# Optimization experiments

Measured on AMD Instinct MI355X. Metric: run time of the kernel, lower is better.

## Reference

```python
import jax, jax.numpy as jnp
import numpy as np

L, DIRS, FEAT, H, B, T = 2, 2, 512, 256, 64, 1024  # layers, directions, feat_dim, per-dir hidden, n_trees, chain_len


def setup_inputs() -> dict:
    key = jax.random.key(0)
    ks = jax.random.split(key, 4)
    s = 0.05
    features = jax.random.normal(ks[0], (B, T, FEAT), jnp.float32)
    Wx = jax.random.normal(ks[1], (L, DIRS, FEAT, 5 * H), jnp.float32) * s
    bx = jnp.zeros((L, DIRS, 5 * H), jnp.float32)
    Wh = jax.random.normal(ks[2], (L, DIRS, H, 5 * H), jnp.float32) * s
    # forget-gate bias slice [2H:3H] initialized to 1.0 as in ChainLSTM
    bh = jnp.zeros((L, DIRS, 5 * H), jnp.float32).at[:, :, 2 * H:3 * H].set(1.0)
    Wp = jax.random.normal(ks[3], (L, DIRS, FEAT, H), jnp.float32) * s
    bp = jnp.zeros((L, DIRS, H), jnp.float32)
    return dict(features=features, Wx=Wx, bx=bx, Wh=Wh, bh=bh, Wp=Wp, bp=bp)


def _run_direction(x, Wx_d, bx_d, Wh_d, bh_d, Wp_d, bp_d, reverse):
    # x: [T, B, F]. Precompute input projections as one big GEMM (memory-bound stream),
    # then scan only carries the tiny [B,H] @ [H,5H] recurrence.
    gx = x @ Wx_d + bx_d          # [T, B, 5H]
    px = x @ Wp_d + bp_d          # [T, B, H] highway projection

    def step(carry, inp):
        c, h = carry
        g, p = inp
        z = g + h @ Wh_d + bh_d
        i, o, f, u, r = jnp.split(z, 5, axis=-1)
        c = jax.nn.sigmoid(i) * jnp.tanh(u) + jax.nn.sigmoid(f) * c
        hh = jax.nn.sigmoid(o) * jnp.tanh(c)
        rg = jax.nn.sigmoid(r)
        hf = rg * hh + (1.0 - rg) * p  # highway gate
        return (c, hf), hf

    zero = jnp.zeros((x.shape[1], bh_d.shape[-1] // 5), x.dtype)
    _, hs = jax.lax.scan(step, (zero, zero), (gx, px), reverse=reverse)
    return hs  # [T, B, H], aligned to original node positions


def reference(features, Wx, bx, Wh, bh, Wp, bp):
    x = jnp.swapaxes(features, 0, 1)  # [T, B, F]
    n_layers = Wx.shape[0]
    for l in range(n_layers):
        outs = []
        for d in range(Wx.shape[1]):  # 0 = foreward, 1 = backward
            hs = _run_direction(x, Wx[l, d], bx[l, d], Wh[l, d], bh[l, d],
                                Wp[l, d], bp[l, d], reverse=(d == 1))
            outs.append(hs)
        x = jnp.concatenate(outs, axis=-1)  # [T, B, 2H] -> next layer input
    return jnp.swapaxes(x, 0, 1)  # [B, T, 2H]
```

## Files before the change

### kernel.cpp

```cpp
#include <hip/hip_runtime.h>
#include <hip/hip_bf16.h>

#define LAYERS 2
#define DIRS   2
#define FEAT   512
#define HDIM   256
#define BATCH  64
#define TLEN   1024
#define FIVEH  1280
#define CHUNK  64
#define NCHUNK (TLEN / CHUNK)
#define NW     8

typedef short bf16x8 __attribute__((ext_vector_type(8)));
typedef float f32x4  __attribute__((ext_vector_type(4)));

__device__ __forceinline__ unsigned short f2bf(float x) {
    unsigned u = __float_as_uint(x);
    unsigned r = (u + 0x7fffu + ((u >> 16) & 1u)) >> 16;
    return (unsigned short)r;
}
__device__ __forceinline__ float bf2f(unsigned short h) {
    return __uint_as_float(((unsigned)h) << 16);
}
__device__ __forceinline__ float sigf(float x) {
    return 1.0f / (1.0f + __expf(-x));
}
__device__ __forceinline__ float tanhfast(float x) {
    return 1.0f - 2.0f / (__expf(2.0f * x) + 1.0f);
}

__global__ __launch_bounds__(256) void castT_kernel(
    const float* __restrict__ src, unsigned short* __restrict__ dst, int K, int N)
{
    __shared__ float tile[32][33];
    const int n0 = blockIdx.x * 32, k0 = blockIdx.y * 32;
    const size_t slab = (size_t)blockIdx.z * K * N;
    src += slab; dst += slab;
    const int tx = threadIdx.x & 31, ty = threadIdx.x >> 5;
    #pragma unroll
    for (int r = 0; r < 32; r += 8)
        tile[ty + r][tx] = src[(size_t)(k0 + ty + r) * N + (n0 + tx)];
    __syncthreads();
    #pragma unroll
    for (int r = 0; r < 32; r += 8)
        dst[(size_t)(n0 + ty + r) * K + (k0 + tx)] = f2bf(tile[tx][ty + r]);
}

__global__ __launch_bounds__(64) void init_kernel(int* __restrict__ flags) {
    if (threadIdx.x < 2 * NW) flags[threadIdx.x * 16] = 0;
}

__global__ __launch_bounds__(256) void proj_kernel(
    const float* __restrict__ features,
    const unsigned short* __restrict__ x1,
    const unsigned short* __restrict__ Wx_t,
    const unsigned short* __restrict__ Wp_t,
    const float* __restrict__ bx, const float* __restrict__ bh,
    const float* __restrict__ bp,
    unsigned short* __restrict__ gx_c,
    unsigned short* __restrict__ px_c,
    int layer, int chunk)
{
    const int ntb = blockIdx.x;
    const int mt  = blockIdx.y;
    const int d   = blockIdx.z;
    const int tid = threadIdx.x;
    const int wave = tid >> 6, lane = tid & 63;

    __shared__ __align__(16) unsigned short Alds[64][40];
    __shared__ __align__(16) unsigned short Blds[64][40];

    const int n0 = ntb * 64;
    const bool isWx = (n0 < FIVEH);
    const unsigned short* Wt = isWx
        ? (Wx_t + ((size_t)(layer * 2 + d) * FIVEH + n0) * FEAT)
        : (Wp_t + ((size_t)(layer * 2 + d) * HDIM + (n0 - FIVEH)) * FEAT);

    const int m0 = mt * 64;
    const int lm = tid >> 2;
    const int lkb = tid & 3;

    const int mrow = m0 + lm;
    const int tl = mrow >> 6;
    const int b  = mrow & 63;
    const int tglob = (d == 0) ? (chunk * CHUNK + tl) : (TLEN - 1 - (chunk * CHUNK + tl));
    const float* Arow0 = features + ((size_t)b * TLEN + tglob) * FEAT;
    const unsigned short* Arow1 = x1 + ((size_t)tglob * BATCH + b) * FEAT;

    f32x4 acc[4];
    #pragma unroll
    for (int i = 0; i < 4; ++i) acc[i] = 0.0f;

    const int fr = lane & 15, quad = lane >> 4;

    for (int k0 = 0; k0 < FEAT; k0 += 32) {
        if (layer == 0) {
            float4 a0 = *(const float4*)(Arow0 + k0 + lkb * 8);
            float4 a1 = *(const float4*)(Arow0 + k0 + lkb * 8 + 4);
            unsigned short* dst = &Alds[lm][lkb * 8];
            dst[0] = f2bf(a0.x); dst[1] = f2bf(a0.y);
            dst[2] = f2bf(a0.z); dst[3] = f2bf(a0.w);
            dst[4] = f2bf(a1.x); dst[5] = f2bf(a1.y);
            dst[6] = f2bf(a1.z); dst[7] = f2bf(a1.w);
        } else {
            uint4 a = *(const uint4*)(Arow1 + k0 + lkb * 8);
            *(uint4*)&Alds[lm][lkb * 8] = a;
        }
        uint4 bv = *(const uint4*)(Wt + (size_t)lm * FEAT + k0 + lkb * 8);
        *(uint4*)&Blds[lm][lkb * 8] = bv;
        __syncthreads();

        bf16x8 af = *(const bf16x8*)&Alds[wave * 16 + fr][quad * 8];
        #pragma unroll
        for (int nt = 0; nt < 4; ++nt) {
            bf16x8 bf = *(const bf16x8*)&Blds[nt * 16 + fr][quad * 8];
            acc[nt] = __builtin_amdgcn_mfma_f32_16x16x32_bf16(af, bf, acc[nt], 0, 0, 0);
        }
        __syncthreads();
    }

    const int ldoff = layer * 2 + d;
    #pragma unroll
    for (int nt = 0; nt < 4; ++nt) {
        const int n = n0 + nt * 16 + fr;
        #pragma unroll
        for (int r = 0; r < 4; ++r) {
            const int m2 = m0 + wave * 16 + quad * 4 + r;
            const int tl2 = m2 >> 6, b2 = m2 & 63;
            float v = acc[nt][r];
            if (n < FIVEH) {
                v += bx[(size_t)ldoff * FIVEH + n] + bh[(size_t)ldoff * FIVEH + n];
                const int g = n >> 8, j = n & 255;
                gx_c[((((size_t)d * CHUNK + tl2) * 5 + g) * HDIM + j) * BATCH + b2] = f2bf(v);
            } else {
                const int j = n - FIVEH;
                v += bp[(size_t)ldoff * HDIM + j];
                px_c[(((size_t)d * CHUNK + tl2) * HDIM + j) * BATCH + b2] = f2bf(v);
            }
        }
    }
}

__global__ __launch_bounds__(256, 1) void recur_kernel(
    const unsigned short* __restrict__ gx_c,
    const unsigned short* __restrict__ px_c,
    const unsigned short* __restrict__ Wh_t,
    unsigned short* __restrict__ x1,
    float* __restrict__ out,
    float* __restrict__ cbuf,
    unsigned short* __restrict__ hbuf,
    int* __restrict__ flags,
    int layer, int chunk)
{
    const int blk = blockIdx.x;
    const int d = blk >> 3, wg = blk & 7;
    const int tid = threadIdx.x;
    const int wave = tid >> 6, lane = tid & 63;
    const int mw = wave >> 1, jh = wave & 1;
    const int col = lane & 15, quad = lane >> 4;
    const int jg = wg * 32 + jh * 16 + col;

    bf16x8 bfr[5][8];
    const unsigned short* Wb = Wh_t + (size_t)(layer * 2 + d) * FIVEH * HDIM;
    #pragma unroll
    for (int g = 0; g < 5; ++g)
        #pragma unroll
        for (int ks = 0; ks < 8; ++ks)
            bfr[g][ks] = *(const bf16x8*)(Wb + (size_t)(g * HDIM + jg) * HDIM + ks * 32 + quad * 8);

    float cst[2][4];
    #pragma unroll
    for (int mt = 0; mt < 2; ++mt)
        #pragma unroll
        for (int r = 0; r < 4; ++r) {
            const int b = (2 * mw + mt) * 16 + quad * 4 + r;
            cst[mt][r] = (chunk == 0) ? 0.0f
                       : cbuf[((size_t)d * BATCH + b) * HDIM + jg];
        }

    const int base = layer * TLEN + chunk * CHUNK;
    int* myflag = &flags[(d * NW + wg) * 16];

    for (int s = 0; s < CHUNK; ++s) {
        const int gs = base + s;

        if (tid < NW) {
            while (__hip_atomic_load(&flags[(d * NW + tid) * 16],
                                     __ATOMIC_RELAXED, __HIP_MEMORY_SCOPE_AGENT) < gs) { }
        }
        __syncthreads();
        __threadfence();

        f32x4 acc[2][5];
        #pragma unroll
        for (int mt = 0; mt < 2; ++mt)
            #pragma unroll
            for (int g = 0; g < 5; ++g) acc[mt][g] = 0.0f;

        if ((gs & (TLEN - 1)) != 0) {
            const unsigned short* hs = hbuf + (size_t)(((gs + 1) & 1) * 2 + d) * BATCH * HDIM;
            bf16x8 af[2][8];
            #pragma unroll
            for (int mt = 0; mt < 2; ++mt)
                #pragma unroll
                for (int ks = 0; ks < 8; ++ks)
                    af[mt][ks] = *(const bf16x8*)(hs + (size_t)((2 * mw + mt) * 16 + col) * HDIM
                                                  + ks * 32 + quad * 8);
            #pragma unroll
            for (int ks = 0; ks < 8; ++ks)
                #pragma unroll
                for (int g = 0; g < 5; ++g) {
                    acc[0][g] = __builtin_amdgcn_mfma_f32_16x16x32_bf16(af[0][ks], bfr[g][ks], acc[0][g], 0, 0, 0);
                    acc[1][g] = __builtin_amdgcn_mfma_f32_16x16x32_bf16(af[1][ks], bfr[g][ks], acc[1][g], 0, 0, 0);
                }
        }

        ushort4 gxv[2][5], pxv[2];
        #pragma unroll
        for (int mt = 0; mt < 2; ++mt) {
            const size_t bb = (2 * mw + mt) * 16 + quad * 4;
            #pragma unroll
            for (int g = 0; g < 5; ++g)
                gxv[mt][g] = *(const ushort4*)(gx_c + ((((size_t)d * CHUNK + s) * 5 + g) * HDIM + jg) * BATCH + bb);
            pxv[mt] = *(const ushort4*)(px_c + (((size_t)d * CHUNK + s) * HDIM + jg) * BATCH + bb);
        }

        const int tpos = chunk * CHUNK + s;
        const int tglob = d ? (TLEN - 1 - tpos) : tpos;
        unsigned short* hdst = hbuf + (size_t)((gs & 1) * 2 + d) * BATCH * HDIM;

        #pragma unroll
        for (int mt = 0; mt < 2; ++mt) {
            const unsigned short* gq0 = (const unsigned short*)&gxv[mt][0];
            const unsigned short* gq1 = (const unsigned short*)&gxv[mt][1];
            const unsigned short* gq2 = (const unsigned short*)&gxv[mt][2];
            const unsigned short* gq3 = (const unsigned short*)&gxv[mt][3];
            const unsigned short* gq4 = (const unsigned short*)&gxv[mt][4];
            const unsigned short* pq  = (const unsigned short*)&pxv[mt];
            #pragma unroll
            for (int r = 0; r < 4; ++r) {
                const float z0 = acc[mt][0][r] + bf2f(gq0[r]);
                const float z1 = acc[mt][1][r] + bf2f(gq1[r]);
                const float z2 = acc[mt][2][r] + bf2f(gq2[r]);
                const float z3 = acc[mt][3][r] + bf2f(gq3[r]);
                const float z4 = acc[mt][4][r] + bf2f(gq4[r]);
                const float p  = bf2f(pq[r]);
                const float ig = sigf(z0);
                const float og = sigf(z1);
                const float fg = sigf(z2);
                const float ug = tanhfast(z3);
                const float rg = sigf(z4);
                const float cc = ig * ug + fg * cst[mt][r];
                cst[mt][r] = cc;
                const float hh = og * tanhfast(cc);
                const float h = rg * hh + (1.0f - rg) * p;
                const int b = (2 * mw + mt) * 16 + quad * 4 + r;
                hdst[(size_t)b * HDIM + jg] = f2bf(h);
                if (layer == 0)
                    x1[((size_t)tglob * BATCH + b) * 512 + d * HDIM + jg] = f2bf(h);
                else
                    out[((size_t)b * TLEN + tglob) * 512 + d * HDIM + jg] = h;
            }
        }

        __syncthreads();
        if (tid == 0) {
            __threadfence();
            __hip_atomic_store(myflag, gs + 1, __ATOMIC_RELAXED, __HIP_MEMORY_SCOPE_AGENT);
        }
    }

    #pragma unroll
    for (int mt = 0; mt < 2; ++mt)
        #pragma unroll
        for (int r = 0; r < 4; ++r) {
            const int b = (2 * mw + mt) * 16 + quad * 4 + r;
            cbuf[((size_t)d * BATCH + b) * HDIM + jg] = cst[mt][r];
        }
}

extern "C" void kernel_launch(void* const* d_in, const int* in_sizes, int n_in,
                              void* d_out, int out_size, void* d_ws, size_t ws_size,
                              hipStream_t stream) {
    const float* features = (const float*)d_in[0];
    const float* Wx = (const float*)d_in[1];
    const float* bx = (const float*)d_in[2];
    const float* Wh = (const float*)d_in[3];
    const float* bh = (const float*)d_in[4];
    const float* Wp = (const float*)d_in[5];
    const float* bp = (const float*)d_in[6];
    float* out = (float*)d_out;

    char* ws = (char*)d_ws;
    size_t off = 0;
    auto alloc = [&](size_t bytes) -> void* {
        void* p = ws + off;
        off += (bytes + 255) & ~(size_t)255;
        return p;
    };
    unsigned short* Wx_t = (unsigned short*)alloc((size_t)LAYERS * DIRS * FIVEH * FEAT * 2);
    unsigned short* Wh_t = (unsigned short*)alloc((size_t)LAYERS * DIRS * FIVEH * HDIM * 2);
    unsigned short* Wp_t = (unsigned short*)alloc((size_t)LAYERS * DIRS * HDIM * FEAT * 2);
    unsigned short* x1   = (unsigned short*)alloc((size_t)TLEN * BATCH * 512 * 2);
    unsigned short* gx_c = (unsigned short*)alloc((size_t)DIRS * CHUNK * BATCH * FIVEH * 2);
    unsigned short* px_c = (unsigned short*)alloc((size_t)DIRS * CHUNK * BATCH * HDIM * 2);
    float* cbuf = (float*)alloc((size_t)DIRS * BATCH * HDIM * 4);
    unsigned short* hbuf = (unsigned short*)alloc((size_t)2 * DIRS * BATCH * HDIM * 2);
    int* flags = (int*)alloc((size_t)2 * NW * 16 * 4);

    init_kernel<<<1, 64, 0, stream>>>(flags);
    castT_kernel<<<dim3(FIVEH / 32, FEAT / 32, 4), 256, 0, stream>>>(Wx, Wx_t, FEAT, FIVEH);
    castT_kernel<<<dim3(FIVEH / 32, HDIM / 32, 4), 256, 0, stream>>>(Wh, Wh_t, HDIM, FIVEH);
    castT_kernel<<<dim3(HDIM / 32, FEAT / 32, 4), 256, 0, stream>>>(Wp, Wp_t, FEAT, HDIM);

    for (int l = 0; l < LAYERS; ++l) {
        for (int c = 0; c < NCHUNK; ++c) {
            proj_kernel<<<dim3(24, 64, 2), 256, 0, stream>>>(
                features, x1, Wx_t, Wp_t, bx, bh, bp, gx_c, px_c, l, c);
            recur_kernel<<<DIRS * NW, 256, 0, stream>>>(
                gx_c, px_c, Wh_t, x1, out, cbuf, hbuf, flags, l, c);
        }
    }
}
```

Measured before the change: 17.65 ms.

## Stage h tile in LDS, publish via atomic stores, hoist gx loads before spin

Each block first writes its bf16 hidden-state slice into a shared-memory tile, then publishes it to the global ping-pong buffer with coalesced 64-bit relaxed atomic stores. The consumer side reads h through atomic loads, and both __threadfence calls are dropped. The gx/px loads are moved ahead of the spin-wait so their latency overlaps the wait. This cuts per-step fence cost and scattered 2-byte global stores, but relies on relaxed agent-scope atomics plus __syncthreads for ordering, which is subtle and could allow stale reads.

```diff
diff --git a/kernel.cpp b/kernel.cpp
--- a/kernel.cpp
+++ b/kernel.cpp
@@ -14,6 +14,9 @@
 
 typedef short bf16x8 __attribute__((ext_vector_type(8)));
 typedef float f32x4  __attribute__((ext_vector_type(4)));
+
+#define ALOAD(p)    __hip_atomic_load((p),      __ATOMIC_RELAXED, __HIP_MEMORY_SCOPE_AGENT)
+#define ASTORE(p,v) __hip_atomic_store((p),(v), __ATOMIC_RELAXED, __HIP_MEMORY_SCOPE_AGENT)
 
 __device__ __forceinline__ unsigned short f2bf(float x) {
     unsigned u = __float_as_uint(x);
@@ -161,6 +164,8 @@
     const int col = lane & 15, quad = lane >> 4;
     const int jg = wg * 32 + jh * 16 + col;
 
+    __shared__ __align__(16) unsigned short hlds[BATCH][32];
+
     bf16x8 bfr[5][8];
     const unsigned short* Wb = Wh_t + (size_t)(layer * 2 + d) * FIVEH * HDIM;
     #pragma unroll
@@ -185,12 +190,20 @@
     for (int s = 0; s < CHUNK; ++s) {
         const int gs = base + s;
 
+        ushort4 gxv[2][5], pxv[2];
+        #pragma unroll
+        for (int mt = 0; mt < 2; ++mt) {
+            const size_t bb = (2 * mw + mt) * 16 + quad * 4;
+            #pragma unroll
+            for (int g = 0; g < 5; ++g)
+                gxv[mt][g] = *(const ushort4*)(gx_c + ((((size_t)d * CHUNK + s) * 5 + g) * HDIM + jg) * BATCH + bb);
+            pxv[mt] = *(const ushort4*)(px_c + (((size_t)d * CHUNK + s) * HDIM + jg) * BATCH + bb);
+        }
+
         if (tid < NW) {
-            while (__hip_atomic_load(&flags[(d * NW + tid) * 16],
-                                     __ATOMIC_RELAXED, __HIP_MEMORY_SCOPE_AGENT) < gs) { }
-        }
-        __syncthreads();
-        __threadfence();
+            while (ALOAD(&flags[(d * NW + tid) * 16]) < gs) { }
+        }
+        __syncthreads();
 
         f32x4 acc[2][5];
         #pragma unroll
@@ -199,14 +212,20 @@
             for (int g = 0; g < 5; ++g) acc[mt][g] = 0.0f;
 
         if ((gs & (TLEN - 1)) != 0) {
-            const unsigned short* hs = hbuf + (size_t)(((gs + 1) & 1) * 2 + d) * BATCH * HDIM;
+            const unsigned long long* hs = (const unsigned long long*)
+                (hbuf + (size_t)(((gs + 1) & 1) * 2 + d) * BATCH * HDIM);
             bf16x8 af[2][8];
             #pragma unroll
             for (int mt = 0; mt < 2; ++mt)
                 #pragma unroll
-                for (int ks = 0; ks < 8; ++ks)
-                    af[mt][ks] = *(const bf16x8*)(hs + (size_t)((2 * mw + mt) * 16 + col) * HDIM
-                                                  + ks * 32 + quad * 8);
+                for (int ks = 0; ks < 8; ++ks) {
+                    const size_t o = ((size_t)((2 * mw + mt) * 16 + col) * HDIM
+                                      + ks * 32 + quad * 8) >> 2;
+                    union { unsigned long long q[2]; bf16x8 v; } u;
+                    u.q[0] = ALOAD(hs + o);
+                    u.q[1] = ALOAD(hs + o + 1);
+                    af[mt][ks] = u.v;
+                }
             #pragma unroll
             for (int ks = 0; ks < 8; ++ks)
                 #pragma unroll
@@ -216,19 +235,8 @@
                 }
         }
 
-        ushort4 gxv[2][5], pxv[2];
-        #pragma unroll
-        for (int mt = 0; mt < 2; ++mt) {
-            const size_t bb = (2 * mw + mt) * 16 + quad * 4;
-            #pragma unroll
-            for (int g = 0; g < 5; ++g)
-                gxv[mt][g] = *(const ushort4*)(gx_c + ((((size_t)d * CHUNK + s) * 5 + g) * HDIM + jg) * BATCH + bb);
-            pxv[mt] = *(const ushort4*)(px_c + (((size_t)d * CHUNK + s) * HDIM + jg) * BATCH + bb);
-        }
-
         const int tpos = chunk * CHUNK + s;
         const int tglob = d ? (TLEN - 1 - tpos) : tpos;
-        unsigned short* hdst = hbuf + (size_t)((gs & 1) * 2 + d) * BATCH * HDIM;
 
         #pragma unroll
         for (int mt = 0; mt < 2; ++mt) {
@@ -256,19 +264,30 @@
                 const float hh = og * tanhfast(cc);
                 const float h = rg * hh + (1.0f - rg) * p;
                 const int b = (2 * mw + mt) * 16 + quad * 4 + r;
-                hdst[(size_t)b * HDIM + jg] = f2bf(h);
+                const unsigned short hb = f2bf(h);
+                hlds[b][jh * 16 + col] = hb;
                 if (layer == 0)
-                    x1[((size_t)tglob * BATCH + b) * 512 + d * HDIM + jg] = f2bf(h);
+                    x1[((size_t)tglob * BATCH + b) * 512 + d * HDIM + jg] = hb;
                 else
                     out[((size_t)b * TLEN + tglob) * 512 + d * HDIM + jg] = h;
             }
         }
 
         __syncthreads();
-        if (tid == 0) {
-            __threadfence();
-            __hip_atomic_store(myflag, gs + 1, __ATOMIC_RELAXED, __HIP_MEMORY_SCOPE_AGENT);
-        }
+
+        {
+            const int b = tid >> 2, jo = (tid & 3) * 8;
+            unsigned long long* hd = (unsigned long long*)
+                (hbuf + (size_t)((gs & 1) * 2 + d) * BATCH * HDIM)
+                + (((size_t)b * HDIM + wg * 32 + jo) >> 2);
+            const unsigned long long* hsv = (const unsigned long long*)&hlds[b][jo];
+            ASTORE(hd,     hsv[0]);
+            ASTORE(hd + 1, hsv[1]);
+        }
+
+        __syncthreads();
+        if (tid == 0)
+            ASTORE(myflag, gs + 1);
     }
 
     #pragma unroll
```

After: 18.95 ms. 1.07x slower.

## Replace flag barrier with step-tagged hidden-state words polled per element

Applied to the files above, without the earlier changes.

Each hidden-state value is now stored as a 32-bit word holding the bf16 value plus the 16-bit step index. Consumers poll those words directly with relaxed atomics until every tag matches the expected step. This removes the per-step flag spin, __syncthreads and thread fences, and lets the gx/px loads be issued before the wait. In exchange the hbuf traffic doubles. A retry guard can fall through and use stale data, and leftover tags from an earlier launch can match the expected step, which makes correctness depend on timing.

```diff
diff --git a/kernel.cpp b/kernel.cpp
--- a/kernel.cpp
+++ b/kernel.cpp
@@ -11,9 +11,14 @@
 #define CHUNK  64
 #define NCHUNK (TLEN / CHUNK)
 #define NW     8
+#define RETRY_GUARD 2048
 
 typedef short bf16x8 __attribute__((ext_vector_type(8)));
 typedef float f32x4  __attribute__((ext_vector_type(4)));
+typedef unsigned long long u64;
+
+#define ALOAD(p)    __hip_atomic_load((p),      __ATOMIC_RELAXED, __HIP_MEMORY_SCOPE_AGENT)
+#define ASTORE(p,v) __hip_atomic_store((p),(v), __ATOMIC_RELAXED, __HIP_MEMORY_SCOPE_AGENT)
 
 __device__ __forceinline__ unsigned short f2bf(float x) {
     unsigned u = __float_as_uint(x);
@@ -45,10 +50,6 @@
     #pragma unroll
     for (int r = 0; r < 32; r += 8)
         dst[(size_t)(n0 + ty + r) * K + (k0 + tx)] = f2bf(tile[tx][ty + r]);
-}
-
-__global__ __launch_bounds__(64) void init_kernel(int* __restrict__ flags) {
-    if (threadIdx.x < 2 * NW) flags[threadIdx.x * 16] = 0;
 }
 
 __global__ __launch_bounds__(256) void proj_kernel(
@@ -149,8 +150,7 @@
     unsigned short* __restrict__ x1,
     float* __restrict__ out,
     float* __restrict__ cbuf,
-    unsigned short* __restrict__ hbuf,
-    int* __restrict__ flags,
+    unsigned int* __restrict__ hbuf,
     int layer, int chunk)
 {
     const int blk = blockIdx.x;
@@ -180,41 +180,9 @@
         }
 
     const int base = layer * TLEN + chunk * CHUNK;
-    int* myflag = &flags[(d * NW + wg) * 16];
 
     for (int s = 0; s < CHUNK; ++s) {
         const int gs = base + s;
-
-        if (tid < NW) {
-            while (__hip_atomic_load(&flags[(d * NW + tid) * 16],
-                                     __ATOMIC_RELAXED, __HIP_MEMORY_SCOPE_AGENT) < gs) { }
-        }
-        __syncthreads();
-        __threadfence();
-
-        f32x4 acc[2][5];
-        #pragma unroll
-        for (int mt = 0; mt < 2; ++mt)
-            #pragma unroll
-            for (int g = 0; g < 5; ++g) acc[mt][g] = 0.0f;
-
-        if ((gs & (TLEN - 1)) != 0) {
-            const unsigned short* hs = hbuf + (size_t)(((gs + 1) & 1) * 2 + d) * BATCH * HDIM;
-            bf16x8 af[2][8];
-            #pragma unroll
-            for (int mt = 0; mt < 2; ++mt)
-                #pragma unroll
-                for (int ks = 0; ks < 8; ++ks)
-                    af[mt][ks] = *(const bf16x8*)(hs + (size_t)((2 * mw + mt) * 16 + col) * HDIM
-                                                  + ks * 32 + quad * 8);
-            #pragma unroll
-            for (int ks = 0; ks < 8; ++ks)
-                #pragma unroll
-                for (int g = 0; g < 5; ++g) {
-                    acc[0][g] = __builtin_amdgcn_mfma_f32_16x16x32_bf16(af[0][ks], bfr[g][ks], acc[0][g], 0, 0, 0);
-                    acc[1][g] = __builtin_amdgcn_mfma_f32_16x16x32_bf16(af[1][ks], bfr[g][ks], acc[1][g], 0, 0, 0);
-                }
-        }
 
         ushort4 gxv[2][5], pxv[2];
         #pragma unroll
@@ -226,10 +194,64 @@
             pxv[mt] = *(const ushort4*)(px_c + (((size_t)d * CHUNK + s) * HDIM + jg) * BATCH + bb);
         }
 
+        f32x4 acc[2][5];
+        #pragma unroll
+        for (int mt = 0; mt < 2; ++mt)
+            #pragma unroll
+            for (int g = 0; g < 5; ++g) acc[mt][g] = 0.0f;
+
+        if ((gs & (TLEN - 1)) != 0) {
+            const unsigned want = (unsigned)(gs - 1);
+            const u64* h64 = (const u64*)(hbuf + (size_t)(((gs + 1) & 1) * 2 + d) * BATCH * HDIM);
+
+            u64 w[2][8][4];
+            #pragma unroll
+            for (int mt = 0; mt < 2; ++mt) {
+                const size_t rb = (size_t)((2 * mw + mt) * 16 + col) * (HDIM / 2) + quad * 4;
+                #pragma unroll
+                for (int ks = 0; ks < 8; ++ks)
+                    #pragma unroll
+                    for (int q = 0; q < 4; ++q)
+                        w[mt][ks][q] = ALOAD(h64 + rb + ks * 16 + q);
+            }
+
+            #pragma unroll
+            for (int ks = 0; ks < 8; ++ks) {
+                #pragma unroll
+                for (int mt = 0; mt < 2; ++mt) {
+                    const u64* ub = h64 + (size_t)((2 * mw + mt) * 16 + col) * (HDIM / 2)
+                                    + quad * 4 + ks * 16;
+                    u64 a0 = w[mt][ks][0], a1 = w[mt][ks][1];
+                    u64 a2 = w[mt][ks][2], a3 = w[mt][ks][3];
+                    int guard = 0;
+                    while (!( ((unsigned)(a0 >> 16) & 0xFFFFu) == want && (unsigned)(a0 >> 48) == want &&
+                              ((unsigned)(a1 >> 16) & 0xFFFFu) == want && (unsigned)(a1 >> 48) == want &&
+                              ((unsigned)(a2 >> 16) & 0xFFFFu) == want && (unsigned)(a2 >> 48) == want &&
+                              ((unsigned)(a3 >> 16) & 0xFFFFu) == want && (unsigned)(a3 >> 48) == want )) {
+                        if (++guard > RETRY_GUARD) break;
+                        a0 = ALOAD(ub + 0); a1 = ALOAD(ub + 1);
+                        a2 = ALOAD(ub + 2); a3 = ALOAD(ub + 3);
+                    }
+                    union { unsigned uw[4]; bf16x8 v; } u;
+                    u.uw[0] = ((unsigned)a0 & 0xFFFFu) | (((unsigned)(a0 >> 32)) << 16);
+                    u.uw[1] = ((unsigned)a1 & 0xFFFFu) | (((unsigned)(a1 >> 32)) << 16);
+                    u.uw[2] = ((unsigned)a2 & 0xFFFFu) | (((unsigned)(a2 >> 32)) << 16);
+                    u.uw[3] = ((unsigned)a3 & 0xFFFFu) | (((unsigned)(a3 >> 32)) << 16);
+                    #pragma unroll
+                    for (int g = 0; g < 5; ++g)
+                        acc[mt][g] = __builtin_amdgcn_mfma_f32_16x16x32_bf16(
+                            u.v, bfr[g][ks], acc[mt][g], 0, 0, 0);
+                }
+            }
+        }
+
         const int tpos = chunk * CHUNK + s;
         const int tglob = d ? (TLEN - 1 - tpos) : tpos;
-        unsigned short* hdst = hbuf + (size_t)((gs & 1) * 2 + d) * BATCH * HDIM;
-
+        const unsigned tagw = (unsigned)gs;
+        unsigned int* hdst = hbuf + (size_t)((gs & 1) * 2 + d) * BATCH * HDIM;
+
+        unsigned short hbv[2][4];
+        float hfv[2][4];
         #pragma unroll
         for (int mt = 0; mt < 2; ++mt) {
             const unsigned short* gq0 = (const unsigned short*)&gxv[mt][0];
@@ -256,19 +278,23 @@
                 const float hh = og * tanhfast(cc);
                 const float h = rg * hh + (1.0f - rg) * p;
                 const int b = (2 * mw + mt) * 16 + quad * 4 + r;
-                hdst[(size_t)b * HDIM + jg] = f2bf(h);
+                const unsigned short hb = f2bf(h);
+                ASTORE(hdst + (size_t)b * HDIM + jg, (tagw << 16) | (unsigned)hb);
+                hbv[mt][r] = hb;
+                hfv[mt][r] = h;
+            }
+        }
+
+        #pragma unroll
+        for (int mt = 0; mt < 2; ++mt)
+            #pragma unroll
+            for (int r = 0; r < 4; ++r) {
+                const int b = (2 * mw + mt) * 16 + quad * 4 + r;
                 if (layer == 0)
-                    x1[((size_t)tglob * BATCH + b) * 512 + d * HDIM + jg] = f2bf(h);
+                    x1[((size_t)tglob * BATCH + b) * 512 + d * HDIM + jg] = hbv[mt][r];
                 else
-                    out[((size_t)b * TLEN + tglob) * 512 + d * HDIM + jg] = h;
-            }
-        }
-
-        __syncthreads();
-        if (tid == 0) {
-            __threadfence();
-            __hip_atomic_store(myflag, gs + 1, __ATOMIC_RELAXED, __HIP_MEMORY_SCOPE_AGENT);
-        }
+                    out[((size_t)b * TLEN + tglob) * 512 + d * HDIM + jg] = hfv[mt][r];
+            }
     }
 
     #pragma unroll
@@ -306,10 +332,8 @@
     unsigned short* gx_c = (unsigned short*)alloc((size_t)DIRS * CHUNK * BATCH * FIVEH * 2);
     unsigned short* px_c = (unsigned short*)alloc((size_t)DIRS * CHUNK * BATCH * HDIM * 2);
     float* cbuf = (float*)alloc((size_t)DIRS * BATCH * HDIM * 4);
-    unsigned short* hbuf = (unsigned short*)alloc((size_t)2 * DIRS * BATCH * HDIM * 2);
-    int* flags = (int*)alloc((size_t)2 * NW * 16 * 4);
-
-    init_kernel<<<1, 64, 0, stream>>>(flags);
+    unsigned int* hbuf = (unsigned int*)alloc((size_t)2 * DIRS * BATCH * HDIM * 4);
+
     castT_kernel<<<dim3(FIVEH / 32, FEAT / 32, 4), 256, 0, stream>>>(Wx, Wx_t, FEAT, FIVEH);
     castT_kernel<<<dim3(FIVEH / 32, HDIM / 32, 4), 256, 0, stream>>>(Wh, Wh_t, HDIM, FIVEH);
     castT_kernel<<<dim3(HDIM / 32, FEAT / 32, 4), 256, 0, stream>>>(Wp, Wp_t, FEAT, HDIM);
@@ -319,7 +343,7 @@
             proj_kernel<<<dim3(24, 64, 2), 256, 0, stream>>>(
                 features, x1, Wx_t, Wp_t, bx, bh, bp, gx_c, px_c, l, c);
             recur_kernel<<<DIRS * NW, 256, 0, stream>>>(
-                gx_c, px_c, Wh_t, x1, out, cbuf, hbuf, flags, l, c);
+                gx_c, px_c, Wh_t, x1, out, cbuf, hbuf, l, c);
         }
     }
 }
```

After: 38.15 ms. 116% more time.
